# Optimization experiments

Hardware: AMD Instinct MI355X
Metric: run time of the kernel (lower is better)

Reference implementation:

```python
import jax, jax.numpy as jnp
import numpy as np

N = 10000      # nodes
E = 160000     # edges
F_IN = 128     # input_dim
HID = 128      # hidden_dim = per-head channels (concat=False)
OUT = 128      # output_dim
H = 4          # heads
L = 4          # layers (all 128->128 here, so params stack)


def setup_inputs() -> dict:
    key = jax.random.key(0)
    ks = jax.random.split(key, 12)
    x = jax.random.normal(ks[0], (N, F_IN), dtype=jnp.float32)
    edge_index = jax.random.randint(ks[1], (2, E), 0, N, dtype=jnp.int64)
    s = 1.0 / np.sqrt(F_IN)
    Wq = jax.random.normal(ks[2], (L, F_IN, H * HID), dtype=jnp.float32) * s
    bq = jnp.zeros((L, H * HID), dtype=jnp.float32)
    Wk = jax.random.normal(ks[3], (L, F_IN, H * HID), dtype=jnp.float32) * s
    bk = jnp.zeros((L, H * HID), dtype=jnp.float32)
    Wv = jax.random.normal(ks[4], (L, F_IN, H * HID), dtype=jnp.float32) * s
    bv = jnp.zeros((L, H * HID), dtype=jnp.float32)
    Wskip = jax.random.normal(ks[5], (L, F_IN, HID), dtype=jnp.float32) * s
    bskip = jnp.zeros((L, HID), dtype=jnp.float32)
    return {"x": x, "edge_index": edge_index, "Wq": Wq, "bq": bq,
            "Wk": Wk, "bk": bk, "Wv": Wv, "bv": bv,
            "Wskip": Wskip, "bskip": bskip}


def _transformer_conv(x, src, dst, Wq, bq, Wk, bk, Wv, bv, Ws, bs):
    # PyG TransformerConv, concat=False (mean over heads), root_weight=True
    n = x.shape[0]
    q = (x @ Wq + bq).reshape(n, H, HID)
    k = (x @ Wk + bk).reshape(n, H, HID)
    v = (x @ Wv + bv).reshape(n, H, HID)
    # per-edge attention logits: [E, H]
    alpha = jnp.einsum('ehc,ehc->eh', q[dst], k[src]) / jnp.sqrt(jnp.float32(HID))
    # segment softmax over destination node
    m = jax.ops.segment_max(alpha, dst, num_segments=n)          # [N, H]
    e = jnp.exp(alpha - m[dst])                                  # [E, H]
    z = jax.ops.segment_sum(e, dst, num_segments=n)              # [N, H]
    a = e / z[dst]                                               # [E, H]
    msg = a[:, :, None] * v[src]                                 # [E, H, C]
    out = jax.ops.segment_sum(msg, dst, num_segments=n)          # [N, H, C]
    out = out.mean(axis=1)                                       # concat=False
    return out + x @ Ws + bs                                     # skip (root_weight)


def reference(x, edge_index, Wq, bq, Wk, bk, Wv, bv, Wskip, bskip):
    src = edge_index[0]
    dst = edge_index[1]
    h = x
    for l in range(L - 1):
        h = _transformer_conv(h, src, dst, Wq[l], bq[l], Wk[l], bk[l],
                              Wv[l], bv[l], Wskip[l], bskip[l])
        h = jax.nn.relu(h)  # dropout p in eval/reference is identity
    h = _transformer_conv(h, src, dst, Wq[-1], bq[-1], Wk[-1], bk[-1],
                          Wv[-1], bv[-1], Wskip[-1], bskip[-1])
    return h
```

## Files before the change

### kernel.cpp

```cpp
#include <hip/hip_runtime.h>
#include <math.h>

static constexpr int F  = 128;
static constexpr int H  = 4;
static constexpr int HF = 512;
static constexpr int NCP = 640;
static constexpr int LAYERS = 4;

typedef __attribute__((ext_vector_type(8))) short bf16x8;
typedef __attribute__((ext_vector_type(4))) float f32x4;

__device__ __forceinline__ unsigned short f2bf(float f) {
    union { float f; unsigned u; } v; v.f = f;
    unsigned r = (v.u + 0x7FFFu + ((v.u >> 16) & 1u)) >> 16;
    return (unsigned short)r;
}
__device__ __forceinline__ float bf2f(unsigned short b) {
    union { unsigned u; float f; } v; v.u = ((unsigned)b) << 16;
    return v.f;
}

__device__ __forceinline__ float row16_sum(float x) {
    int t;
    t = __builtin_amdgcn_update_dpp(0, __float_as_int(x), 0xB1, 0xF, 0xF, true);
    x += __int_as_float(t);
    t = __builtin_amdgcn_update_dpp(0, __float_as_int(x), 0x4E, 0xF, 0xF, true);
    x += __int_as_float(t);
    t = __builtin_amdgcn_update_dpp(0, __float_as_int(x), 0x124, 0xF, 0xF, true);
    x += __int_as_float(t);
    t = __builtin_amdgcn_update_dpp(0, __float_as_int(x), 0x128, 0xF, 0xF, true);
    x += __int_as_float(t);
    return x;
}

__global__ void hist_kernel(const int* __restrict__ dst, int* __restrict__ deg, int E) {
    int e = blockIdx.x * blockDim.x + threadIdx.x;
    if (e < E) atomicAdd(&deg[dst[e]], 1);
}

__global__ void scan_kernel(const int* __restrict__ deg, int* __restrict__ row_ptr, int n) {
    __shared__ int wsum[16];
    __shared__ int carry_s, wtot_s;
    const int tid = threadIdx.x;
    const int lane = tid & 63;
    const int wid = tid >> 6;
    if (tid == 0) { carry_s = 0; row_ptr[0] = 0; }
    __syncthreads();
    for (int base = 0; base < n; base += 1024) {
        int i = base + tid;
        int x = (i < n) ? deg[i] : 0;
#pragma unroll
        for (int off = 1; off < 64; off <<= 1) {
            int t = __shfl_up(x, off, 64);
            if (lane >= off) x += t;
        }
        if (lane == 63) wsum[wid] = x;
        __syncthreads();
        if (tid == 0) {
            int s = 0;
#pragma unroll
            for (int j = 0; j < 16; ++j) { int t = wsum[j]; wsum[j] = s; s += t; }
            wtot_s = s;
        }
        __syncthreads();
        int incl = x + wsum[wid] + carry_s;
        if (i < n) row_ptr[i + 1] = incl;
        __syncthreads();
        if (tid == 0) carry_s += wtot_s;
        __syncthreads();
    }
}

__global__ void scatter_kernel(const int* __restrict__ src, const int* __restrict__ dst,
                               const int* __restrict__ row_ptr, int* __restrict__ cursor,
                               int* __restrict__ csr_src, int E) {
    int e = blockIdx.x * blockDim.x + threadIdx.x;
    if (e < E) {
        int d = dst[e];
        int pos = atomicAdd(&cursor[d], 1);
        csr_src[row_ptr[d] + pos] = src[e];
    }
}

static constexpr int NB_CONV  = 1250;
static constexpr int NB_WQK   = 64;
static constexpr int NB_WS    = 64;
static constexpr int NB_BPOST = 256;
static constexpr int NB_BIAS  = LAYERS;
static constexpr int NB_PREP  = NB_CONV + NB_WQK + NB_WS + NB_BPOST + NB_BIAS;

__global__ __launch_bounds__(256) void prep_kernel(
    const float* __restrict__ x, unsigned short* __restrict__ h_bf, int n4,
    const float* __restrict__ Wq, const float* __restrict__ Wk,
    const float* __restrict__ Wv, const float* __restrict__ Ws,
    const float* __restrict__ bq, const float* __restrict__ bs, const float* __restrict__ bv,
    unsigned short* __restrict__ Bpre, unsigned short* __restrict__ Bpost,
    float* __restrict__ biasPre, float* __restrict__ biasPost, float scale)
{
    __shared__ __attribute__((aligned(16))) float smem[64 * 33 * 2];
    const int tid = threadIdx.x;
    int b = blockIdx.x;

    if (b < NB_CONV) {
        int i = b * 256 + tid;
        if (i < n4) {
            float4 v = *(const float4*)(x + (size_t)i * 4);
            ushort4 o;
            o.x = f2bf(v.x); o.y = f2bf(v.y); o.z = f2bf(v.z); o.w = f2bf(v.w);
            *(ushort4*)(h_bf + (size_t)i * 4) = o;
        }
        return;
    }
    b -= NB_CONV;
    if (b < NB_WQK) {
        float (*As)[33] = (float (*)[33])smem;
        float (*Bs)[33] = (float (*)[33])(smem + 64 * 33);
        const int bx = b & 1, by = (b >> 1) & 1, lh = b >> 2;
        const int l = lh >> 2, h = lh & 3;
        const int c0 = by * 64, k0 = bx * 64;
        const float* Ab = Wk + (size_t)l * 65536 + h * 128;
        const float* Bb = Wq + (size_t)l * 65536 + h * 128;
        const int tx = tid & 15, ty = tid >> 4;
        float acc[4][4] = {};
        for (int jj = 0; jj < 128; jj += 32) {
#pragma unroll
            for (int rep = 0; rep < 2; ++rep) {
                int f = tid + rep * 256;
                int r = f >> 3, j4 = (f & 7) * 4;
                float4 a = *(const float4*)(Ab + (size_t)(c0 + r) * 512 + jj + j4);
                As[r][j4 + 0] = a.x; As[r][j4 + 1] = a.y; As[r][j4 + 2] = a.z; As[r][j4 + 3] = a.w;
                float4 bb = *(const float4*)(Bb + (size_t)(k0 + r) * 512 + jj + j4);
                Bs[r][j4 + 0] = bb.x; Bs[r][j4 + 1] = bb.y; Bs[r][j4 + 2] = bb.z; Bs[r][j4 + 3] = bb.w;
            }
            __syncthreads();
#pragma unroll
            for (int j = 0; j < 32; ++j) {
                float a0 = As[ty * 4 + 0][j], a1 = As[ty * 4 + 1][j];
                float a2 = As[ty * 4 + 2][j], a3 = As[ty * 4 + 3][j];
                float b0 = Bs[tx * 4 + 0][j], b1 = Bs[tx * 4 + 1][j];
                float b2 = Bs[tx * 4 + 2][j], b3 = Bs[tx * 4 + 3][j];
                acc[0][0] += a0 * b0; acc[0][1] += a0 * b1; acc[0][2] += a0 * b2; acc[0][3] += a0 * b3;
                acc[1][0] += a1 * b0; acc[1][1] += a1 * b1; acc[1][2] += a1 * b2; acc[1][3] += a1 * b3;
                acc[2][0] += a2 * b0; acc[2][1] += a2 * b1; acc[2][2] += a2 * b2; acc[2][3] += a2 * b3;
                acc[3][0] += a3 * b0; acc[3][1] += a3 * b1; acc[3][2] += a3 * b2; acc[3][3] += a3 * b3;
            }
            __syncthreads();
        }
#pragma unroll
        for (int i = 0; i < 4; ++i)
#pragma unroll
            for (int t = 0; t < 4; ++t) {
                int c = c0 + ty * 4 + i;
                int k = k0 + tx * 4 + t;
                Bpre[(size_t)l * NCP * 128 + (size_t)(h * 128 + c) * 128 + k] = f2bf(scale * acc[i][t]);
            }
        return;
    }
    b -= NB_WQK;
    if (b < NB_WS) {
        unsigned short (*t)[33] = (unsigned short (*)[33])smem;
        const int bx = b & 3, by = (b >> 2) & 3, l = b >> 4;
        const int k0 = bx * 32, n0 = by * 32;
        const int cx = tid & 31, ry = tid >> 5;
#pragma unroll
        for (int rr = 0; rr < 32; rr += 8) {
            int k = k0 + ry + rr;
            t[ry + rr][cx] = f2bf(Ws[(size_t)l * 16384 + (size_t)k * 128 + n0 + cx]);
        }
        __syncthreads();
#pragma unroll
        for (int rr = 0; rr < 32; rr += 8) {
            int n = n0 + ry + rr;
            Bpre[(size_t)l * NCP * 128 + (size_t)(512 + n) * 128 + k0 + cx] = t[cx][ry + rr];
        }
        return;
    }
    b -= NB_WS;
    if (b < NB_BPOST) {
        unsigned short (*t)[33] = (unsigned short (*)[33])smem;
        const int bx = b & 3, by = (b >> 2) & 3, lh = b >> 4;
        const int l = lh >> 2, h = lh & 3;
        const int ci0 = bx * 32, co0 = by * 32;
        const int cx = tid & 31, ry = tid >> 5;
#pragma unroll
        for (int rr = 0; rr < 32; rr += 8) {
            int ci = ci0 + ry + rr;
            t[ry + rr][cx] = f2bf(0.25f * Wv[(size_t)l * 65536 + (size_t)ci * 512 + h * 128 + co0 + cx]);
        }
        __syncthreads();
#pragma unroll
        for (int rr = 0; rr < 32; rr += 8) {
            int co = co0 + ry + rr;
            Bpost[(size_t)l * 65536 + (size_t)co * 512 + h * 128 + ci0 + cx] = t[cx][ry + rr];
        }
        return;
    }
    b -= NB_BPOST;
    {
        const int l = b;
        for (int n = tid; n < NCP; n += 256) {
            float v;
            if (n < 512) {
                int h = n >> 7, c = n & 127;
                float s = 0.f;
                for (int j = 0; j < 128; ++j)
                    s += bq[(size_t)l * 512 + h * 128 + j] * Wk[(size_t)l * 65536 + (size_t)c * 512 + h * 128 + j];
                v = s * scale;
            } else {
                v = bs[(size_t)l * 128 + (n - 512)];
            }
            biasPre[(size_t)l * NCP + n] = v;
        }
        for (int c = tid; c < 128; c += 256) {
            float s = 0.f;
            for (int h = 0; h < 4; ++h) s += bv[(size_t)l * 512 + h * 128 + c];
            biasPost[(size_t)l * 128 + c] = 0.25f * s;
        }
    }
}

__global__ __launch_bounds__(256) void gemm_pre(
    const unsigned short* __restrict__ Abf,
    const unsigned short* __restrict__ Bt,
    const float* __restrict__ bias,
    unsigned short* __restrict__ Qt,
    float* __restrict__ Sb,
    int M)
{
    __shared__ unsigned short As[128][72];
    __shared__ unsigned short Bs[128][72];

    const int tid = threadIdx.x;
    const int wave = tid >> 6, lane = tid & 63;
    const int lane16 = lane & 15, quad = lane >> 4;
    const int wr = wave >> 1, wc = wave & 1;
    const int row0 = blockIdx.y * 128;
    const int col0 = blockIdx.x * 128;

    f32x4 acc[4][4] = {};

    for (int kk = 0; kk < 128; kk += 64) {
#pragma unroll
        for (int j = 0; j < 4; ++j) {
            int c = tid + j * 256;
            int r = c >> 3, c8 = (c & 7) * 8;
            bf16x8 v = {};
            if (row0 + r < M) v = *(const bf16x8*)(Abf + (size_t)(row0 + r) * 128 + kk + c8);
            *(bf16x8*)&As[r][c8] = v;
        }
#pragma unroll
        for (int j = 0; j < 4; ++j) {
            int c = tid + j * 256;
            int r = c >> 3, c8 = (c & 7) * 8;
            *(bf16x8*)&Bs[r][c8] = *(const bf16x8*)(Bt + (size_t)(col0 + r) * 128 + kk + c8);
        }
        __syncthreads();

#pragma unroll
        for (int ks = 0; ks < 2; ++ks) {
            bf16x8 a[4], b[4];
#pragma unroll
            for (int i = 0; i < 4; ++i)
                a[i] = *(const bf16x8*)&As[wr * 64 + i * 16 + lane16][ks * 32 + quad * 8];
#pragma unroll
            for (int i = 0; i < 4; ++i)
                b[i] = *(const bf16x8*)&Bs[wc * 64 + i * 16 + lane16][ks * 32 + quad * 8];
#pragma unroll
            for (int mi = 0; mi < 4; ++mi)
#pragma unroll
                for (int ni = 0; ni < 4; ++ni)
                    acc[mi][ni] = __builtin_amdgcn_mfma_f32_16x16x32_bf16(
                        a[mi], b[ni], acc[mi][ni], 0, 0, 0);
        }
        __syncthreads();
    }

#pragma unroll
    for (int mi = 0; mi < 4; ++mi) {
        int rowb = row0 + wr * 64 + mi * 16 + quad * 4;
#pragma unroll
        for (int ni = 0; ni < 4; ++ni) {
            int col = col0 + wc * 64 + ni * 16 + lane16;
            float bv = bias[col];
#pragma unroll
            for (int r = 0; r < 4; ++r) {
                int gr = rowb + r;
                if (gr < M) {
                    float v = acc[mi][ni][r] + bv;
                    if (col < 512) Qt[(size_t)gr * 512 + col] = f2bf(v);
                    else           Sb[(size_t)gr * 128 + (col - 512)] = v;
                }
            }
        }
    }
}

__global__ __launch_bounds__(128, 4) void attn_agg(
    const unsigned short* __restrict__ Qt,
    const unsigned short* __restrict__ Hb,
    const int* __restrict__ row_ptr,
    const int* __restrict__ csr_src,
    unsigned short* __restrict__ Agg,
    int N)
{
    __shared__ float part[4][16][10];

    const int tid = threadIdx.x;
    const int wv  = tid >> 6;
    const int g   = (tid >> 4) & 3;
    const int l16 = tid & 15;
    const int node = blockIdx.x;

    const float NEG = -3e38f;

    float qf[8];
    {
        bf16x8 qv = *(const bf16x8*)(Qt + (size_t)node * HF + g * F + l16 * 8);
#pragma unroll
        for (int j = 0; j < 8; ++j) qf[j] = bf2f((unsigned short)qv[j]);
    }
    const unsigned short* Hl = Hb + (size_t)l16 * 8;

    const int beg = row_ptr[node];
    const int end = row_ptr[node + 1];

    float m = NEG, z = 0.f;
    float acc[8];
#pragma unroll
    for (int j = 0; j < 8; ++j) acc[j] = 0.f;

    const int begw = beg + wv * 4;
    if (begw < end) {
        const int last = end - 1;
        const int NB = (end - begw + 7) >> 3;

#define CLD(i) csr_src[(i) < last ? (i) : last]

        int a0 = CLD(begw + 0), a1 = CLD(begw + 1), a2 = CLD(begw + 2), a3 = CLD(begw + 3);
        bf16x8 hA0 = *(const bf16x8*)(Hl + (size_t)a0 * F);
        bf16x8 hA1 = *(const bf16x8*)(Hl + (size_t)a1 * F);
        bf16x8 hA2 = *(const bf16x8*)(Hl + (size_t)a2 * F);
        bf16x8 hA3 = *(const bf16x8*)(Hl + (size_t)a3 * F);
        int b0 = CLD(begw + 8), b1 = CLD(begw + 9), b2 = CLD(begw + 10), b3 = CLD(begw + 11);
        bf16x8 hB0 = *(const bf16x8*)(Hl + (size_t)b0 * F);
        bf16x8 hB1 = *(const bf16x8*)(Hl + (size_t)b1 * F);
        bf16x8 hB2 = *(const bf16x8*)(Hl + (size_t)b2 * F);
        bf16x8 hB3 = *(const bf16x8*)(Hl + (size_t)b3 * F);
        a0 = CLD(begw + 16); a1 = CLD(begw + 17); a2 = CLD(begw + 18); a3 = CLD(begw + 19);
        b0 = CLD(begw + 24); b1 = CLD(begw + 25); b2 = CLD(begw + 26); b3 = CLD(begw + 27);
        __builtin_amdgcn_sched_barrier(0);

#define ATTN_BATCH(H0, H1, H2, H3, I0, I1, I2, I3)                              \
    {                                                                           \
        float hf[4][8];                                                         \
        _Pragma("unroll")                                                       \
        for (int j = 0; j < 8; ++j) {                                           \
            hf[0][j] = bf2f((unsigned short)H0[j]);                             \
            hf[1][j] = bf2f((unsigned short)H1[j]);                             \
            hf[2][j] = bf2f((unsigned short)H2[j]);                             \
            hf[3][j] = bf2f((unsigned short)H3[j]);                             \
        }                                                                       \
        if (k + 2 < NB) {                                                       \
            H0 = *(const bf16x8*)(Hl + (size_t)I0 * F);                         \
            H1 = *(const bf16x8*)(Hl + (size_t)I1 * F);                         \
            H2 = *(const bf16x8*)(Hl + (size_t)I2 * F);                         \
            H3 = *(const bf16x8*)(Hl + (size_t)I3 * F);                         \
            I0 = CLD(base + 32); I1 = CLD(base + 33);                           \
            I2 = CLD(base + 34); I3 = CLD(base + 35);                           \
        }                                                                       \
        __builtin_amdgcn_sched_barrier(0);   \
        float p0 = 0.f, p1 = 0.f, p2 = 0.f, p3 = 0.f;                           \
        _Pragma("unroll")                                                       \
        for (int j = 0; j < 8; ++j) {                                           \
            p0 += qf[j] * hf[0][j]; p1 += qf[j] * hf[1][j];                     \
            p2 += qf[j] * hf[2][j]; p3 += qf[j] * hf[3][j];                     \
        }                                                                       \
        p0 = row16_sum(p0); p1 = row16_sum(p1);                                 \
        p2 = row16_sum(p2); p3 = row16_sum(p3);                                 \
        const int nv = end - base;                                              \
        if (nv < 4) { if (nv < 2) p1 = NEG; if (nv < 3) p2 = NEG; p3 = NEG; }   \
        float bm = fmaxf(fmaxf(p0, p1), fmaxf(p2, p3));                         \
        float mn = fmaxf(m, bm);                                                \
        float rs = exp2f(m - mn);                                               \
        float w0 = exp2f(p0 - mn), w1 = exp2f(p1 - mn);                         \
        float w2 = exp2f(p2 - mn), w3 = exp2f(p3 - mn);                         \
        z = z * rs + (w0 + w1) + (w2 + w3);                                     \
        _Pragma("unroll")                                                       \
        for (int j = 0; j < 8; ++j)                                             \
            acc[j] = acc[j] * rs + w0 * hf[0][j] + w1 * hf[1][j]                \
                   + w2 * hf[2][j] + w3 * hf[3][j];                             \
        m = mn;                                                                 \
    }

        int base = begw;
        int k = 0;
        for (;;) {
            ATTN_BATCH(hA0, hA1, hA2, hA3, a0, a1, a2, a3)
            ++k; base += 8;
            if (k >= NB) break;
            ATTN_BATCH(hB0, hB1, hB2, hB3, b0, b1, b2, b3)
            ++k; base += 8;
            if (k >= NB) break;
        }
#undef ATTN_BATCH
#undef CLD
    }

    if (wv == 1) {
#pragma unroll
        for (int j = 0; j < 8; ++j) part[g][l16][j] = acc[j];
        part[g][l16][8] = m;
        part[g][l16][9] = z;
    }
    __syncthreads();
    if (wv == 0) {
        float om = part[g][l16][8];
        float oz = part[g][l16][9];
        float M  = fmaxf(m, om);
        float sa = exp2f(m - M);
        float sb = exp2f(om - M);
        float zz = z * sa + oz * sb;
        float inv = (zz > 0.f) ? 1.f / zz : 0.f;
        bf16x8 o;
#pragma unroll
        for (int j = 0; j < 8; ++j)
            o[j] = (short)f2bf((acc[j] * sa + part[g][l16][j] * sb) * inv);
        *(bf16x8*)(Agg + (size_t)node * HF + g * F + l16 * 8) = o;
    }
}

__global__ __launch_bounds__(256) void gemm_post(
    const unsigned short* __restrict__ Agg,
    const unsigned short* __restrict__ Bt,
    const float* __restrict__ bias,
    const float* __restrict__ Sb,
    float* __restrict__ out_f,
    unsigned short* __restrict__ out_bf,
    int relu, int M)
{
    __shared__ unsigned short As[64][72];
    __shared__ unsigned short Bs[64][72];

    const int tid = threadIdx.x;
    const int wave = tid >> 6, lane = tid & 63;
    const int lane16 = lane & 15, quad = lane >> 4;
    const int row0 = blockIdx.y * 64;
    const int col0 = blockIdx.x * 64;

    f32x4 acc[4] = {};

    for (int kk = 0; kk < 512; kk += 64) {
#pragma unroll
        for (int rep = 0; rep < 2; ++rep) {
            int c = tid + rep * 256;
            int r = c >> 3, c8 = (c & 7) * 8;
            bf16x8 v = {};
            if (row0 + r < M) v = *(const bf16x8*)(Agg + (size_t)(row0 + r) * 512 + kk + c8);
            *(bf16x8*)&As[r][c8] = v;
            *(bf16x8*)&Bs[r][c8] = *(const bf16x8*)(Bt + (size_t)(col0 + r) * 512 + kk + c8);
        }
        __syncthreads();

#pragma unroll
        for (int ks = 0; ks < 2; ++ks) {
            bf16x8 b = *(const bf16x8*)&Bs[wave * 16 + lane16][ks * 32 + quad * 8];
#pragma unroll
            for (int mt = 0; mt < 4; ++mt) {
                bf16x8 a = *(const bf16x8*)&As[mt * 16 + lane16][ks * 32 + quad * 8];
                acc[mt] = __builtin_amdgcn_mfma_f32_16x16x32_bf16(a, b, acc[mt], 0, 0, 0);
            }
        }
        __syncthreads();
    }

    const int col = col0 + wave * 16 + lane16;
    const float bcol = bias[col];
#pragma unroll
    for (int mt = 0; mt < 4; ++mt) {
#pragma unroll
        for (int r = 0; r < 4; ++r) {
            int row = row0 + mt * 16 + quad * 4 + r;
            if (row < M) {
                float v = acc[mt][r] + bcol + Sb[(size_t)row * 128 + col];
                if (relu) v = fmaxf(v, 0.f);
                if (out_f)  out_f[(size_t)row * 128 + col] = v;
                if (out_bf) out_bf[(size_t)row * 128 + col] = f2bf(v);
            }
        }
    }
}

extern "C" void kernel_launch(void* const* d_in, const int* in_sizes, int n_in,
                              void* d_out, int out_size, void* d_ws, size_t ws_size,
                              hipStream_t stream) {
    const float* x     = (const float*)d_in[0];
    const int*   ei    = (const int*)d_in[1];
    const float* Wq    = (const float*)d_in[2];
    const float* bq    = (const float*)d_in[3];
    const float* Wk    = (const float*)d_in[4];
    const float* bk    = (const float*)d_in[5];
    const float* Wv    = (const float*)d_in[6];
    const float* bv    = (const float*)d_in[7];
    const float* Wskip = (const float*)d_in[8];
    const float* bskip = (const float*)d_in[9];
    float* out = (float*)d_out;
    (void)bk;

    const int N = in_sizes[0] / F;
    const int E = in_sizes[1] / 2;
    const float scale = 0.08838834764831845f * 1.4426950408889634f;

    const int* src = ei;
    const int* dst = ei + E;

    char* p = (char*)d_ws;
    float* Sb       = (float*)p;               p += (size_t)N * F * sizeof(float);
    float* biasPreP = (float*)p;               p += (size_t)LAYERS * NCP * sizeof(float);
    float* biasPostP= (float*)p;               p += (size_t)LAYERS * 128 * sizeof(float);
    unsigned short* h_bf  = (unsigned short*)p; p += (size_t)N * F * sizeof(unsigned short);
    unsigned short* Qt    = (unsigned short*)p; p += (size_t)N * HF * sizeof(unsigned short);
    unsigned short* AggB  = (unsigned short*)p; p += (size_t)N * HF * sizeof(unsigned short);
    unsigned short* BpreP = (unsigned short*)p; p += (size_t)LAYERS * NCP * 128 * sizeof(unsigned short);
    unsigned short* BpostP= (unsigned short*)p; p += (size_t)LAYERS * 128 * 512 * sizeof(unsigned short);
    int* deg     = (int*)p;                    p += (size_t)N * sizeof(int);
    int* cursor  = (int*)p;                    p += (size_t)N * sizeof(int);
    int* row_ptr = (int*)p;                    p += (size_t)(N + 1) * sizeof(int);
    int* csr_src = (int*)p;

    hipMemsetAsync(deg, 0, 2 * (size_t)N * sizeof(int), stream);
    {
        int blocks = (E + 255) / 256;
        hist_kernel<<<blocks, 256, 0, stream>>>(dst, deg, E);
        scan_kernel<<<1, 1024, 0, stream>>>(deg, row_ptr, N);
        scatter_kernel<<<blocks, 256, 0, stream>>>(src, dst, row_ptr, cursor, csr_src, E);
    }

    prep_kernel<<<NB_PREP, 256, 0, stream>>>(x, h_bf, N * F / 4,
                                             Wq, Wk, Wv, Wskip,
                                             bq, bskip, bv,
                                             BpreP, BpostP, biasPreP, biasPostP, scale);

    const int rowBlocks128 = (N + 127) / 128;
    const int rowBlocks64  = (N + 63) / 64;

    for (int l = 0; l < LAYERS; ++l) {
        dim3 gridPre(NCP / 128, rowBlocks128);
        gemm_pre<<<gridPre, 256, 0, stream>>>(h_bf,
                                              BpreP + (size_t)l * NCP * 128,
                                              biasPreP + (size_t)l * NCP,
                                              Qt, Sb, N);

        attn_agg<<<N, 128, 0, stream>>>(Qt, h_bf, row_ptr, csr_src, AggB, N);

        float* out_f = nullptr;
        unsigned short* out_bf = nullptr;
        int relu;
        if (l == LAYERS - 1) { out_f = out; relu = 0; }
        else { out_bf = h_bf; relu = 1; }

        dim3 gridPost(2, rowBlocks64);
        gemm_post<<<gridPost, 256, 0, stream>>>(AggB,
                                                BpostP + (size_t)l * 128 * 512,
                                                biasPostP + (size_t)l * 128,
                                                Sb, out_f, out_bf, relu, N);
    }
}
```

Baseline: 264.2 us.

## Fold skip projection into post-aggregation GEMM as extra K slice

The skip-connection matmul x@Ws moves out of the pre-GEMM, which used to write an fp32 Sb buffer, and into the post-GEMM as an extra 128-wide K chunk over the current bf16 hidden state. Its bias is merged into the post bias. The hidden state is now double-buffered so the post-GEMM can read the layer input while writing the next one. This removes the fp32 Sb write and read and one column block of the pre-GEMM, at the cost of more K iterations and a branchy loader in gemm_post.

```diff
diff --git a/kernel.cpp b/kernel.cpp
--- a/kernel.cpp
+++ b/kernel.cpp
@@ -198,23 +198,17 @@
     b -= NB_BPOST;
     {
         const int l = b;
-        for (int n = tid; n < NCP; n += 256) {
-            float v;
-            if (n < 512) {
-                int h = n >> 7, c = n & 127;
-                float s = 0.f;
-                for (int j = 0; j < 128; ++j)
-                    s += bq[(size_t)l * 512 + h * 128 + j] * Wk[(size_t)l * 65536 + (size_t)c * 512 + h * 128 + j];
-                v = s * scale;
-            } else {
-                v = bs[(size_t)l * 128 + (n - 512)];
-            }
-            biasPre[(size_t)l * NCP + n] = v;
+        for (int n = tid; n < 512; n += 256) {
+            int h = n >> 7, c = n & 127;
+            float s = 0.f;
+            for (int j = 0; j < 128; ++j)
+                s += bq[(size_t)l * 512 + h * 128 + j] * Wk[(size_t)l * 65536 + (size_t)c * 512 + h * 128 + j];
+            biasPre[(size_t)l * NCP + n] = s * scale;
         }
         for (int c = tid; c < 128; c += 256) {
             float s = 0.f;
             for (int h = 0; h < 4; ++h) s += bv[(size_t)l * 512 + h * 128 + c];
-            biasPost[(size_t)l * 128 + c] = 0.25f * s;
+            biasPost[(size_t)l * 128 + c] = 0.25f * s + bs[(size_t)l * 128 + c];
         }
     }
 }
@@ -224,7 +218,6 @@
     const unsigned short* __restrict__ Bt,
     const float* __restrict__ bias,
     unsigned short* __restrict__ Qt,
-    float* __restrict__ Sb,
     int M)
 {
     __shared__ unsigned short As[128][72];
@@ -285,11 +278,7 @@
 #pragma unroll
             for (int r = 0; r < 4; ++r) {
                 int gr = rowb + r;
-                if (gr < M) {
-                    float v = acc[mi][ni][r] + bv;
-                    if (col < 512) Qt[(size_t)gr * 512 + col] = f2bf(v);
-                    else           Sb[(size_t)gr * 128 + (col - 512)] = v;
-                }
+                if (gr < M) Qt[(size_t)gr * 512 + col] = f2bf(acc[mi][ni][r] + bv);
             }
         }
     }
@@ -431,9 +420,10 @@
 
 __global__ __launch_bounds__(256) void gemm_post(
     const unsigned short* __restrict__ Agg,
+    const unsigned short* __restrict__ Hc,
     const unsigned short* __restrict__ Bt,
+    const unsigned short* __restrict__ Bsk,
     const float* __restrict__ bias,
-    const float* __restrict__ Sb,
     float* __restrict__ out_f,
     unsigned short* __restrict__ out_bf,
     int relu, int M)
@@ -449,15 +439,21 @@
 
     f32x4 acc[4] = {};
 
-    for (int kk = 0; kk < 512; kk += 64) {
+    for (int kk = 0; kk < 640; kk += 64) {
+        const bool sk = kk >= 512;
+        const int k0 = sk ? kk - 512 : kk;
 #pragma unroll
         for (int rep = 0; rep < 2; ++rep) {
             int c = tid + rep * 256;
             int r = c >> 3, c8 = (c & 7) * 8;
             bf16x8 v = {};
-            if (row0 + r < M) v = *(const bf16x8*)(Agg + (size_t)(row0 + r) * 512 + kk + c8);
+            if (row0 + r < M)
+                v = sk ? *(const bf16x8*)(Hc  + (size_t)(row0 + r) * 128 + k0 + c8)
+                       : *(const bf16x8*)(Agg + (size_t)(row0 + r) * 512 + k0 + c8);
             *(bf16x8*)&As[r][c8] = v;
-            *(bf16x8*)&Bs[r][c8] = *(const bf16x8*)(Bt + (size_t)(col0 + r) * 512 + kk + c8);
+            *(bf16x8*)&Bs[r][c8] = sk
+                ? *(const bf16x8*)(Bsk + (size_t)(col0 + r) * 128 + k0 + c8)
+                : *(const bf16x8*)(Bt  + (size_t)(col0 + r) * 512 + k0 + c8);
         }
         __syncthreads();
 
@@ -481,7 +477,7 @@
         for (int r = 0; r < 4; ++r) {
             int row = row0 + mt * 16 + quad * 4 + r;
             if (row < M) {
-                float v = acc[mt][r] + bcol + Sb[(size_t)row * 128 + col];
+                float v = acc[mt][r] + bcol;
                 if (relu) v = fmaxf(v, 0.f);
                 if (out_f)  out_f[(size_t)row * 128 + col] = v;
                 if (out_bf) out_bf[(size_t)row * 128 + col] = f2bf(v);
@@ -514,10 +510,10 @@
     const int* dst = ei + E;
 
     char* p = (char*)d_ws;
-    float* Sb       = (float*)p;               p += (size_t)N * F * sizeof(float);
     float* biasPreP = (float*)p;               p += (size_t)LAYERS * NCP * sizeof(float);
     float* biasPostP= (float*)p;               p += (size_t)LAYERS * 128 * sizeof(float);
-    unsigned short* h_bf  = (unsigned short*)p; p += (size_t)N * F * sizeof(unsigned short);
+    unsigned short* h0    = (unsigned short*)p; p += (size_t)N * F * sizeof(unsigned short);
+    unsigned short* h1    = (unsigned short*)p; p += (size_t)N * F * sizeof(unsigned short);
     unsigned short* Qt    = (unsigned short*)p; p += (size_t)N * HF * sizeof(unsigned short);
     unsigned short* AggB  = (unsigned short*)p; p += (size_t)N * HF * sizeof(unsigned short);
     unsigned short* BpreP = (unsigned short*)p; p += (size_t)LAYERS * NCP * 128 * sizeof(unsigned short);
@@ -535,7 +531,7 @@
         scatter_kernel<<<blocks, 256, 0, stream>>>(src, dst, row_ptr, cursor, csr_src, E);
     }
 
-    prep_kernel<<<NB_PREP, 256, 0, stream>>>(x, h_bf, N * F / 4,
+    prep_kernel<<<NB_PREP, 256, 0, stream>>>(x, h0, N * F / 4,
                                              Wq, Wk, Wv, Wskip,
                                              bq, bskip, bv,
                                              BpreP, BpostP, biasPreP, biasPostP, scale);
@@ -543,25 +539,30 @@
     const int rowBlocks128 = (N + 127) / 128;
     const int rowBlocks64  = (N + 63) / 64;
 
+    unsigned short* hcur = h0;
+    unsigned short* hnxt = h1;
     for (int l = 0; l < LAYERS; ++l) {
-        dim3 gridPre(NCP / 128, rowBlocks128);
-        gemm_pre<<<gridPre, 256, 0, stream>>>(h_bf,
+        dim3 gridPre(4, rowBlocks128);
+        gemm_pre<<<gridPre, 256, 0, stream>>>(hcur,
                                               BpreP + (size_t)l * NCP * 128,
                                               biasPreP + (size_t)l * NCP,
-                                              Qt, Sb, N);
-
-        attn_agg<<<N, 128, 0, stream>>>(Qt, h_bf, row_ptr, csr_src, AggB, N);
+                                              Qt, N);
+
+        attn_agg<<<N, 128, 0, stream>>>(Qt, hcur, row_ptr, csr_src, AggB, N);
 
         float* out_f = nullptr;
         unsigned short* out_bf = nullptr;
         int relu;
         if (l == LAYERS - 1) { out_f = out; relu = 0; }
-        else { out_bf = h_bf; relu = 1; }
+        else { out_bf = hnxt; relu = 1; }
 
         dim3 gridPost(2, rowBlocks64);
-        gemm_post<<<gridPost, 256, 0, stream>>>(AggB,
+        gemm_post<<<gridPost, 256, 0, stream>>>(AggB, hcur,
                                                 BpostP + (size_t)l * 128 * 512,
+                                                BpreP + (size_t)l * NCP * 128 + (size_t)512 * 128,
                                                 biasPostP + (size_t)l * 128,
-                                                Sb, out_f, out_bf, relu, N);
-    }
-}
+                                                out_f, out_bf, relu, N);
+
+        unsigned short* t = hcur; hcur = hnxt; hnxt = t;
+    }
+}
```

Measured after the change: 254.1 us. -3.9%, faster.
